# Kernel tuning notes

Hardware: AMD Instinct MI355X
Metric: run time of the kernel (lower is better)

## Reference

```python
import jax, jax.numpy as jnp
import numpy as np

N_NODES = 25000
IN_DIM = 16
EDGE_DIM = 8
HID = 32
OUT_DIM = 16
N_EDGES = 400000
MLP_HID = 32


def setup_inputs() -> dict:
    key = jax.random.key(0)
    ks = jax.random.split(key, 12)
    x = jax.random.normal(ks[0], (N_NODES, IN_DIM), dtype=jnp.float32)
    edge_index = jax.random.randint(ks[1], (2, N_EDGES), 0, N_NODES, dtype=jnp.int32)
    edge_attr = jax.random.normal(ks[2], (N_EDGES, EDGE_DIM), dtype=jnp.float32)
    s = lambda fan_in: 1.0 / np.sqrt(fan_in)
    W1 = jax.random.uniform(ks[3], (EDGE_DIM, MLP_HID), minval=-s(EDGE_DIM), maxval=s(EDGE_DIM))
    b1 = jax.random.uniform(ks[4], (MLP_HID,), minval=-s(EDGE_DIM), maxval=s(EDGE_DIM))
    W2 = jax.random.uniform(ks[5], (MLP_HID, IN_DIM * HID), minval=-s(MLP_HID), maxval=s(MLP_HID))
    b2 = jax.random.uniform(ks[6], (IN_DIM * HID,), minval=-s(MLP_HID), maxval=s(MLP_HID))
    root = jax.random.uniform(ks[7], (IN_DIM, HID), minval=-s(IN_DIM), maxval=s(IN_DIM))
    bias = jnp.zeros((HID,), dtype=jnp.float32)
    Wlin = jax.random.uniform(ks[8], (HID, OUT_DIM), minval=-s(HID), maxval=s(HID))
    blin = jax.random.uniform(ks[9], (OUT_DIM,), minval=-s(HID), maxval=s(HID))
    return {"x": x, "edge_attr": edge_attr, "W1": W1, "b1": b1, "W2": W2,
            "b2": b2, "root": root, "bias": bias, "Wlin": Wlin, "blin": blin,
            "edge_index": edge_index}


def reference(x, edge_attr, W1, b1, W2, b2, root, bias, Wlin, blin, edge_index):
    src, dst = edge_index[0], edge_index[1]  # x_j gathered from src, aggregated at dst
    # edge MLP -> per-edge weight matrix [E, IN_DIM, HID]
    h = jax.nn.relu(edge_attr @ W1 + b1)
    W_e = (h @ W2 + b2).reshape(-1, IN_DIM, HID)
    # gather source features and per-edge matvec: [E, HID]
    msg = jnp.einsum('ei,eio->eo', x[src], W_e)
    # scatter-mean over target nodes
    agg = jax.ops.segment_sum(msg, dst, num_segments=N_NODES)
    cnt = jax.ops.segment_sum(jnp.ones((msg.shape[0],), dtype=msg.dtype), dst, num_segments=N_NODES)
    agg = agg / jnp.maximum(cnt, 1.0)[:, None]
    # NNConv root weight + bias, then ReLU and final linear
    out = jax.nn.relu(agg + x @ root + bias)
    return out @ Wlin + blin
```

## Files before the change

### kernel.cpp

```cpp
#include <hip/hip_runtime.h>
#include <cstdint>

#define E_EDGES 400000
#define N_NODES 25000
#define NG      25000
#define NPACK   18432
#define EBLOCKS 782
#define NWAVES_E (EBLOCKS*4)

typedef float f32x4 __attribute__((ext_vector_type(4)));
typedef __bf16 bf16x8 __attribute__((ext_vector_type(8)));

static __device__ __forceinline__ ushort f2bf(float f) {
    union { __bf16 b; ushort u; } c; c.b = (__bf16)f; return c.u;
}

__global__ void __launch_bounds__(256) k_pack(const float* __restrict__ W2,
                                              const float* __restrict__ b2,
                                              const float* __restrict__ W1,
                                              const int* __restrict__ ei,
                                              ushort* __restrict__ packed,
                                              uint* __restrict__ cnt_u) {
    int t = blockIdx.x * 256 + threadIdx.x;
    if (t < NPACK) {
        float v = 0.0f;
        if (t < 17408) {
            int j  = t & 7;
            int ln = (t >> 3) & 15;
            int kg = (t >> 7) & 3;
            int nt = (t >> 9) & 1;
            int kt = t >> 10;
            int kap = (j < 4) ? (kg * 4 + j) : (16 + kg * 4 + (j - 4));
            if (kt < 16)       v = W2[kap * 512 + kt * 32 + nt * 16 + ln];
            else if (kap < 16) v = b2[kap * 32 + nt * 16 + ln];
        } else {
            int idx  = t - 17408;
            int half = idx >> 9;
            int lane = (idx >> 3) & 63;
            int j    = idx & 7;
            int kg = lane >> 4, ln = lane & 15;
            if (kg == 0) v = W1[j * 32 + half * 16 + ln];
        }
        packed[t] = f2bf(v);
    }
    if (t < E_EDGES) atomicAdd(&cnt_u[ei[E_EDGES + t]], 1u);
}

__global__ void __launch_bounds__(256, 2) k_edge(const float* __restrict__ ea,
                                                 const float* __restrict__ x,
                                                 const int* __restrict__ ei,
                                                 const ushort* __restrict__ packed,
                                                 const float* __restrict__ b1,
                                                 float* __restrict__ agg) {
    const int lane = threadIdx.x & 63;
    const int ln = lane & 15;
    const int kg = lane >> 4;
    const int wid = blockIdx.x * 4 + (threadIdx.x >> 6);

    bf16x8 wfr[34];
#pragma unroll
    for (int i = 0; i < 34; ++i)
        wfr[i] = *(const bf16x8*)(packed + (size_t)i * 512 + (size_t)lane * 8);
    const bf16x8 aw0 = *(const bf16x8*)(packed + 17408 + (size_t)lane * 8);
    const bf16x8 aw1 = *(const bf16x8*)(packed + 17408 + 512 + (size_t)lane * 8);
    const f32x4 blo4 = *(const f32x4*)(b1 + 4 * kg);
    const f32x4 bhi4 = *(const f32x4*)(b1 + 16 + 4 * kg);

    const f32x4 z4 = {0.f, 0.f, 0.f, 0.f};
    const __bf16 zb = (__bf16)0.0f;

    int g = wid;
    f32x4 ea0, ea1, xq0, xq1, xq2, xq3;
    {
        const int s0 = ei[g * 16 + ln];
        const f32x4* ep = (const f32x4*)(ea + (size_t)(g * 16 + ln) * 8);
        ea0 = ep[0]; ea1 = ep[1];
        const f32x4* xp = (const f32x4*)(x + (size_t)s0 * 16);
        xq0 = xp[0]; xq1 = xp[1]; xq2 = xp[2]; xq3 = xp[3];
    }

    while (true) {
        const int gn = g + NWAVES_E;
        const bool pf = gn < NG;

        int ns0 = 0;
        f32x4 nea0 = z4, nea1 = z4;
        if (pf) {
            ns0 = ei[gn * 16 + ln];
            const f32x4* nep = (const f32x4*)(ea + (size_t)(gn * 16 + ln) * 8);
            nea0 = nep[0]; nea1 = nep[1];
        }
        const int4 d4 = *(const int4*)(ei + E_EDGES + g * 16 + kg * 4);

        bf16x8 eb;
        if (kg == 0) {
            eb[0]=(__bf16)ea0[0]; eb[1]=(__bf16)ea0[1]; eb[2]=(__bf16)ea0[2]; eb[3]=(__bf16)ea0[3];
            eb[4]=(__bf16)ea1[0]; eb[5]=(__bf16)ea1[1]; eb[6]=(__bf16)ea1[2]; eb[7]=(__bf16)ea1[3];
        } else {
            eb[0]=zb; eb[1]=zb; eb[2]=zb; eb[3]=zb; eb[4]=zb; eb[5]=zb; eb[6]=zb; eb[7]=zb;
        }
        const f32x4 hA0 = __builtin_amdgcn_mfma_f32_16x16x32_bf16(aw0, eb, z4, 0, 0, 0);
        const f32x4 hA1 = __builtin_amdgcn_mfma_f32_16x16x32_bf16(aw1, eb, z4, 0, 0, 0);

        float h[8];
#pragma unroll
        for (int r = 0; r < 4; ++r) {
            h[r]     = fmaxf(hA0[r] + blo4[r], 0.f);
            h[4 + r] = fmaxf(hA1[r] + bhi4[r], 0.f);
        }

        float xr[16];
        xr[0]=xq0[0]; xr[1]=xq0[1]; xr[2]=xq0[2]; xr[3]=xq0[3];
        xr[4]=xq1[0]; xr[5]=xq1[1]; xr[6]=xq1[2]; xr[7]=xq1[3];
        xr[8]=xq2[0]; xr[9]=xq2[1]; xr[10]=xq2[2]; xr[11]=xq2[3];
        xr[12]=xq3[0]; xr[13]=xq3[1]; xr[14]=xq3[2]; xr[15]=xq3[3];

        f32x4 acc0 = z4, acc1 = z4;

#pragma unroll
        for (int kt = 0; kt < 8; ++kt) {
            const float xv = xr[kt];
            bf16x8 a;
#pragma unroll
            for (int j = 0; j < 8; ++j) a[j] = (__bf16)(xv * h[j]);
            acc0 = __builtin_amdgcn_mfma_f32_16x16x32_bf16(a, wfr[kt * 2 + 0], acc0, 0, 0, 0);
            acc1 = __builtin_amdgcn_mfma_f32_16x16x32_bf16(a, wfr[kt * 2 + 1], acc1, 0, 0, 0);
        }

        f32x4 nx0 = z4, nx1 = z4, nx2 = z4, nx3 = z4;
        if (pf) {
            const f32x4* nxp = (const f32x4*)(x + (size_t)ns0 * 16);
            nx0 = nxp[0]; nx1 = nxp[1]; nx2 = nxp[2]; nx3 = nxp[3];
        }

#pragma unroll
        for (int kt = 8; kt < 16; ++kt) {
            const float xv = xr[kt];
            bf16x8 a;
#pragma unroll
            for (int j = 0; j < 8; ++j) a[j] = (__bf16)(xv * h[j]);
            acc0 = __builtin_amdgcn_mfma_f32_16x16x32_bf16(a, wfr[kt * 2 + 0], acc0, 0, 0, 0);
            acc1 = __builtin_amdgcn_mfma_f32_16x16x32_bf16(a, wfr[kt * 2 + 1], acc1, 0, 0, 0);
        }
        {
            const f32x4 xs = (kg == 0) ? xq0 : ((kg == 1) ? xq1 : ((kg == 2) ? xq2 : xq3));
            bf16x8 a;
            a[0]=(__bf16)xs[0]; a[1]=(__bf16)xs[1]; a[2]=(__bf16)xs[2]; a[3]=(__bf16)xs[3];
            a[4]=zb; a[5]=zb; a[6]=zb; a[7]=zb;
            acc0 = __builtin_amdgcn_mfma_f32_16x16x32_bf16(a, wfr[32], acc0, 0, 0, 0);
            acc1 = __builtin_amdgcn_mfma_f32_16x16x32_bf16(a, wfr[33], acc1, 0, 0, 0);
        }

        atomicAdd(&agg[d4.x * 32 + ln],      acc0[0]);
        atomicAdd(&agg[d4.y * 32 + ln],      acc0[1]);
        atomicAdd(&agg[d4.z * 32 + ln],      acc0[2]);
        atomicAdd(&agg[d4.w * 32 + ln],      acc0[3]);
        atomicAdd(&agg[d4.x * 32 + 16 + ln], acc1[0]);
        atomicAdd(&agg[d4.y * 32 + 16 + ln], acc1[1]);
        atomicAdd(&agg[d4.z * 32 + 16 + ln], acc1[2]);
        atomicAdd(&agg[d4.w * 32 + 16 + ln], acc1[3]);

        if (!pf) break;
        g = gn;
        ea0 = nea0; ea1 = nea1;
        xq0 = nx0; xq1 = nx1; xq2 = nx2; xq3 = nx3;
    }
}

__global__ void __launch_bounds__(256) k_node(const float* __restrict__ agg,
                                              const uint* __restrict__ cnt_u,
                                              const float* __restrict__ x,
                                              const float* __restrict__ root,
                                              const float* __restrict__ bias,
                                              const float* __restrict__ Wlin,
                                              const float* __restrict__ blin,
                                              float* __restrict__ out) {
    __shared__ float al[256];
    const int n0 = blockIdx.x * 8;
    const int t = threadIdx.x;
    const int n = n0 + (t >> 5), h = t & 31;
    float a = 0.0f;
    if (n < N_NODES) {
        const float c = (float)cnt_u[n];
        float s = agg[n * 32 + h] / fmaxf(c, 1.0f) + bias[h];
        const f32x4* xp = (const f32x4*)(x + (size_t)n * 16);
        const f32x4 x0 = xp[0], x1 = xp[1], x2 = xp[2], x3 = xp[3];
        float xv[16];
        xv[0]=x0[0]; xv[1]=x0[1]; xv[2]=x0[2]; xv[3]=x0[3];
        xv[4]=x1[0]; xv[5]=x1[1]; xv[6]=x1[2]; xv[7]=x1[3];
        xv[8]=x2[0]; xv[9]=x2[1]; xv[10]=x2[2]; xv[11]=x2[3];
        xv[12]=x3[0]; xv[13]=x3[1]; xv[14]=x3[2]; xv[15]=x3[3];
#pragma unroll
        for (int i = 0; i < 16; ++i) s += xv[i] * root[i * 32 + h];
        a = fmaxf(s, 0.0f);
    }
    al[t] = a;
    __syncthreads();
    if (t < 128) {
        const int nj = n0 + (t >> 4), j = t & 15;
        if (nj < N_NODES) {
            float s = blin[j];
#pragma unroll
            for (int h2 = 0; h2 < 32; ++h2) s += al[(t >> 4) * 32 + h2] * Wlin[h2 * 16 + j];
            out[nj * 16 + j] = s;
        }
    }
}

extern "C" void kernel_launch(void* const* d_in, const int* in_sizes, int n_in,
                              void* d_out, int out_size, void* d_ws, size_t ws_size,
                              hipStream_t stream) {
    const float* x    = (const float*)d_in[0];
    const float* ea   = (const float*)d_in[1];
    const float* W1   = (const float*)d_in[2];
    const float* b1   = (const float*)d_in[3];
    const float* W2   = (const float*)d_in[4];
    const float* b2   = (const float*)d_in[5];
    const float* root = (const float*)d_in[6];
    const float* bias = (const float*)d_in[7];
    const float* Wlin = (const float*)d_in[8];
    const float* blin = (const float*)d_in[9];
    const int*   ei   = (const int*)d_in[10];
    float* out = (float*)d_out;

    char* ws = (char*)d_ws;
    float*  agg    = (float*)(ws + 0);
    uint*   cnt_u  = (uint*)(ws + 3200000);
    ushort* packed = (ushort*)(ws + 3300000);

    hipMemsetAsync(d_ws, 0, 3300000, stream);

    k_pack<<<1563, 256, 0, stream>>>(W2, b2, W1, ei, packed, cnt_u);
    k_edge<<<EBLOCKS, 256, 0, stream>>>(ea, x, ei, packed, b1, agg);
    k_node<<<3125, 256, 0, stream>>>(agg, cnt_u, x, root, bias, Wlin, blin, out);
}
```

Before: 87.18 us.

## Switch edge kernel to 32x32x16 MFMA with LDS-resident packed weights

Reworks the edge kernel so each wave handles 32 edges per iteration using 32x32x16 bf16 MFMAs instead of pairs of 16x16x32 MFMAs over 16 edges. The packed W2/b2 fragments now sit in shared memory instead of 34 register-held fragments, and the source-index prefetch is deepened by one more iteration. The aim is to cut MFMA instruction count, relieve register pressure, and hide gather latency better. In exchange it adds LDS reads inside the inner loop and a per-block LDS fill, changes the block count and launch bounds, and needs a matching repack of the weights.

```diff
diff --git a/kernel.cpp b/kernel.cpp
--- a/kernel.cpp
+++ b/kernel.cpp
@@ -3,12 +3,16 @@
 
 #define E_EDGES 400000
 #define N_NODES 25000
-#define NG      25000
-#define NPACK   18432
-#define EBLOCKS 782
-#define NWAVES_E (EBLOCKS*4)
-
-typedef float f32x4 __attribute__((ext_vector_type(4)));
+#define NG32    12500
+#define NTILES  33
+#define NPACKB  (NTILES*64*8)
+#define NPACKA  512
+#define NPACKT  (NPACKB+NPACKA)
+#define EBLOCKS 1042
+#define ESTRIDE (EBLOCKS*4)
+
+typedef float  f32x4  __attribute__((ext_vector_type(4)));
+typedef float  f32x16 __attribute__((ext_vector_type(16)));
 typedef __bf16 bf16x8 __attribute__((ext_vector_type(8)));
 
 static __device__ __forceinline__ ushort f2bf(float f) {
@@ -22,92 +26,118 @@
                                               ushort* __restrict__ packed,
                                               uint* __restrict__ cnt_u) {
     int t = blockIdx.x * 256 + threadIdx.x;
-    if (t < NPACK) {
+    if (t < NPACKT) {
         float v = 0.0f;
-        if (t < 17408) {
-            int j  = t & 7;
-            int ln = (t >> 3) & 15;
-            int kg = (t >> 7) & 3;
-            int nt = (t >> 9) & 1;
-            int kt = t >> 10;
-            int kap = (j < 4) ? (kg * 4 + j) : (16 + kg * 4 + (j - 4));
-            if (kt < 16)       v = W2[kap * 512 + kt * 32 + nt * 16 + ln];
-            else if (kap < 16) v = b2[kap * 32 + nt * 16 + ln];
+        if (t < NPACKB) {
+            int j = t & 7, lane = (t >> 3) & 63, kt = t >> 9;
+            int o = lane & 31, hi = lane >> 5;
+            if (kt < 32) {
+                int i = kt >> 1, p = kt & 1;
+                int m = (j & 3) + 8 * (2 * p + (j >> 2)) + 4 * hi;
+                v = W2[m * 512 + i * 32 + o];
+            } else {
+                int k = hi * 8 + j;
+                v = b2[k * 32 + o];
+            }
         } else {
-            int idx  = t - 17408;
-            int half = idx >> 9;
-            int lane = (idx >> 3) & 63;
-            int j    = idx & 7;
-            int kg = lane >> 4, ln = lane & 15;
-            if (kg == 0) v = W1[j * 32 + half * 16 + ln];
+            int t2 = t - NPACKB;
+            int j = t2 & 7, lane = t2 >> 3;
+            int m = lane & 31, hi = lane >> 5;
+            if (hi == 0) v = W1[j * 32 + m];
         }
         packed[t] = f2bf(v);
     }
     if (t < E_EDGES) atomicAdd(&cnt_u[ei[E_EDGES + t]], 1u);
 }
 
-__global__ void __launch_bounds__(256, 2) k_edge(const float* __restrict__ ea,
-                                                 const float* __restrict__ x,
-                                                 const int* __restrict__ ei,
-                                                 const ushort* __restrict__ packed,
-                                                 const float* __restrict__ b1,
-                                                 float* __restrict__ agg) {
+__global__ void __launch_bounds__(256) k_edge(const float* __restrict__ ea,
+                                              const float* __restrict__ x,
+                                              const int* __restrict__ ei,
+                                              const ushort* __restrict__ packed,
+                                              const float* __restrict__ b1,
+                                              float* __restrict__ agg) {
+    __shared__ alignas(16) ushort bl[NPACKB];
+    {
+        const uint4* s = (const uint4*)packed;
+        uint4* d = (uint4*)bl;
+        for (int i = threadIdx.x; i < NPACKB / 8; i += 256) d[i] = s[i];
+    }
+    __syncthreads();
+
     const int lane = threadIdx.x & 63;
-    const int ln = lane & 15;
-    const int kg = lane >> 4;
+    const int o  = lane & 31;
+    const int hi = lane >> 5;
     const int wid = blockIdx.x * 4 + (threadIdx.x >> 6);
 
-    bf16x8 wfr[34];
-#pragma unroll
-    for (int i = 0; i < 34; ++i)
-        wfr[i] = *(const bf16x8*)(packed + (size_t)i * 512 + (size_t)lane * 8);
-    const bf16x8 aw0 = *(const bf16x8*)(packed + 17408 + (size_t)lane * 8);
-    const bf16x8 aw1 = *(const bf16x8*)(packed + 17408 + 512 + (size_t)lane * 8);
-    const f32x4 blo4 = *(const f32x4*)(b1 + 4 * kg);
-    const f32x4 bhi4 = *(const f32x4*)(b1 + 16 + 4 * kg);
-
-    const f32x4 z4 = {0.f, 0.f, 0.f, 0.f};
+    const bf16x8 aw = *(const bf16x8*)(packed + NPACKB + (size_t)lane * 8);
+    const f32x4 b1q0 = *(const f32x4*)(b1 + 0  + 4 * hi);
+    const f32x4 b1q1 = *(const f32x4*)(b1 + 8  + 4 * hi);
+    const f32x4 b1q2 = *(const f32x4*)(b1 + 16 + 4 * hi);
+    const f32x4 b1q3 = *(const f32x4*)(b1 + 24 + 4 * hi);
+
+    const f32x16 z16 = {0.f,0.f,0.f,0.f,0.f,0.f,0.f,0.f,0.f,0.f,0.f,0.f,0.f,0.f,0.f,0.f};
+    const f32x4  z4  = {0.f,0.f,0.f,0.f};
     const __bf16 zb = (__bf16)0.0f;
 
     int g = wid;
     f32x4 ea0, ea1, xq0, xq1, xq2, xq3;
+    int s_nxt = 0;
     {
-        const int s0 = ei[g * 16 + ln];
-        const f32x4* ep = (const f32x4*)(ea + (size_t)(g * 16 + ln) * 8);
+        const int e = g * 32 + o;
+        const int s_cur = ei[e];
+        const f32x4* ep = (const f32x4*)(ea + (size_t)e * 8);
         ea0 = ep[0]; ea1 = ep[1];
-        const f32x4* xp = (const f32x4*)(x + (size_t)s0 * 16);
+        const f32x4* xp = (const f32x4*)(x + (size_t)s_cur * 16);
         xq0 = xp[0]; xq1 = xp[1]; xq2 = xp[2]; xq3 = xp[3];
+        const int gnx = g + ESTRIDE;
+        if (gnx < NG32) s_nxt = ei[gnx * 32 + o];
     }
 
     while (true) {
-        const int gn = g + NWAVES_E;
-        const bool pf = gn < NG;
-
-        int ns0 = 0;
-        f32x4 nea0 = z4, nea1 = z4;
+        const int gn = g + ESTRIDE;
+        const bool pf = gn < NG32;
+
+        f32x4 nea0 = z4, nea1 = z4, nx0 = z4, nx1 = z4, nx2 = z4, nx3 = z4;
+        int s_nn = 0;
         if (pf) {
-            ns0 = ei[gn * 16 + ln];
-            const f32x4* nep = (const f32x4*)(ea + (size_t)(gn * 16 + ln) * 8);
+            const f32x4* nep = (const f32x4*)(ea + (size_t)(gn * 32 + o) * 8);
             nea0 = nep[0]; nea1 = nep[1];
-        }
-        const int4 d4 = *(const int4*)(ei + E_EDGES + g * 16 + kg * 4);
+            const f32x4* nxp = (const f32x4*)(x + (size_t)s_nxt * 16);
+            nx0 = nxp[0]; nx1 = nxp[1]; nx2 = nxp[2]; nx3 = nxp[3];
+            const int gnn = gn + ESTRIDE;
+            if (gnn < NG32) s_nn = ei[gnn * 32 + o];
+        }
+        const int4 dq0 = *(const int4*)(ei + E_EDGES + g * 32 + 0  + 4 * hi);
+        const int4 dq1 = *(const int4*)(ei + E_EDGES + g * 32 + 8  + 4 * hi);
+        const int4 dq2 = *(const int4*)(ei + E_EDGES + g * 32 + 16 + 4 * hi);
+        const int4 dq3 = *(const int4*)(ei + E_EDGES + g * 32 + 24 + 4 * hi);
 
         bf16x8 eb;
-        if (kg == 0) {
+        if (hi == 0) {
             eb[0]=(__bf16)ea0[0]; eb[1]=(__bf16)ea0[1]; eb[2]=(__bf16)ea0[2]; eb[3]=(__bf16)ea0[3];
             eb[4]=(__bf16)ea1[0]; eb[5]=(__bf16)ea1[1]; eb[6]=(__bf16)ea1[2]; eb[7]=(__bf16)ea1[3];
         } else {
             eb[0]=zb; eb[1]=zb; eb[2]=zb; eb[3]=zb; eb[4]=zb; eb[5]=zb; eb[6]=zb; eb[7]=zb;
         }
-        const f32x4 hA0 = __builtin_amdgcn_mfma_f32_16x16x32_bf16(aw0, eb, z4, 0, 0, 0);
-        const f32x4 hA1 = __builtin_amdgcn_mfma_f32_16x16x32_bf16(aw1, eb, z4, 0, 0, 0);
-
-        float h[8];
-#pragma unroll
-        for (int r = 0; r < 4; ++r) {
-            h[r]     = fmaxf(hA0[r] + blo4[r], 0.f);
-            h[4 + r] = fmaxf(hA1[r] + bhi4[r], 0.f);
-        }
+        const f32x16 hC = __builtin_amdgcn_mfma_f32_32x32x16_bf16(aw, eb, z16, 0, 0, 0);
+
+        float hreg[16];
+        hreg[0]  = fmaxf(hC[0]  + b1q0[0], 0.f);
+        hreg[1]  = fmaxf(hC[1]  + b1q0[1], 0.f);
+        hreg[2]  = fmaxf(hC[2]  + b1q0[2], 0.f);
+        hreg[3]  = fmaxf(hC[3]  + b1q0[3], 0.f);
+        hreg[4]  = fmaxf(hC[4]  + b1q1[0], 0.f);
+        hreg[5]  = fmaxf(hC[5]  + b1q1[1], 0.f);
+        hreg[6]  = fmaxf(hC[6]  + b1q1[2], 0.f);
+        hreg[7]  = fmaxf(hC[7]  + b1q1[3], 0.f);
+        hreg[8]  = fmaxf(hC[8]  + b1q2[0], 0.f);
+        hreg[9]  = fmaxf(hC[9]  + b1q2[1], 0.f);
+        hreg[10] = fmaxf(hC[10] + b1q2[2], 0.f);
+        hreg[11] = fmaxf(hC[11] + b1q2[3], 0.f);
+        hreg[12] = fmaxf(hC[12] + b1q3[0], 0.f);
+        hreg[13] = fmaxf(hC[13] + b1q3[1], 0.f);
+        hreg[14] = fmaxf(hC[14] + b1q3[2], 0.f);
+        hreg[15] = fmaxf(hC[15] + b1q3[3], 0.f);
 
         float xr[16];
         xr[0]=xq0[0]; xr[1]=xq0[1]; xr[2]=xq0[2]; xr[3]=xq0[3];
@@ -115,55 +145,48 @@
         xr[8]=xq2[0]; xr[9]=xq2[1]; xr[10]=xq2[2]; xr[11]=xq2[3];
         xr[12]=xq3[0]; xr[13]=xq3[1]; xr[14]=xq3[2]; xr[15]=xq3[3];
 
-        f32x4 acc0 = z4, acc1 = z4;
-
-#pragma unroll
-        for (int kt = 0; kt < 8; ++kt) {
-            const float xv = xr[kt];
+        f32x16 acc = z16;
+
+#pragma unroll
+        for (int kt = 0; kt < 32; ++kt) {
+            const int p = kt & 1;
+            const float xv = xr[kt >> 1];
             bf16x8 a;
 #pragma unroll
-            for (int j = 0; j < 8; ++j) a[j] = (__bf16)(xv * h[j]);
-            acc0 = __builtin_amdgcn_mfma_f32_16x16x32_bf16(a, wfr[kt * 2 + 0], acc0, 0, 0, 0);
-            acc1 = __builtin_amdgcn_mfma_f32_16x16x32_bf16(a, wfr[kt * 2 + 1], acc1, 0, 0, 0);
-        }
-
-        f32x4 nx0 = z4, nx1 = z4, nx2 = z4, nx3 = z4;
-        if (pf) {
-            const f32x4* nxp = (const f32x4*)(x + (size_t)ns0 * 16);
-            nx0 = nxp[0]; nx1 = nxp[1]; nx2 = nxp[2]; nx3 = nxp[3];
-        }
-
-#pragma unroll
-        for (int kt = 8; kt < 16; ++kt) {
-            const float xv = xr[kt];
+            for (int j = 0; j < 8; ++j) a[j] = (__bf16)(xv * hreg[p * 8 + j]);
+            const bf16x8 bf = *(const bf16x8*)(&bl[kt * 512 + lane * 8]);
+            acc = __builtin_amdgcn_mfma_f32_32x32x16_bf16(a, bf, acc, 0, 0, 0);
+        }
+        {
             bf16x8 a;
 #pragma unroll
-            for (int j = 0; j < 8; ++j) a[j] = (__bf16)(xv * h[j]);
-            acc0 = __builtin_amdgcn_mfma_f32_16x16x32_bf16(a, wfr[kt * 2 + 0], acc0, 0, 0, 0);
-            acc1 = __builtin_amdgcn_mfma_f32_16x16x32_bf16(a, wfr[kt * 2 + 1], acc1, 0, 0, 0);
-        }
-        {
-            const f32x4 xs = (kg == 0) ? xq0 : ((kg == 1) ? xq1 : ((kg == 2) ? xq2 : xq3));
-            bf16x8 a;
-            a[0]=(__bf16)xs[0]; a[1]=(__bf16)xs[1]; a[2]=(__bf16)xs[2]; a[3]=(__bf16)xs[3];
-            a[4]=zb; a[5]=zb; a[6]=zb; a[7]=zb;
-            acc0 = __builtin_amdgcn_mfma_f32_16x16x32_bf16(a, wfr[32], acc0, 0, 0, 0);
-            acc1 = __builtin_amdgcn_mfma_f32_16x16x32_bf16(a, wfr[33], acc1, 0, 0, 0);
-        }
-
-        atomicAdd(&agg[d4.x * 32 + ln],      acc0[0]);
-        atomicAdd(&agg[d4.y * 32 + ln],      acc0[1]);
-        atomicAdd(&agg[d4.z * 32 + ln],      acc0[2]);
-        atomicAdd(&agg[d4.w * 32 + ln],      acc0[3]);
-        atomicAdd(&agg[d4.x * 32 + 16 + ln], acc1[0]);
-        atomicAdd(&agg[d4.y * 32 + 16 + ln], acc1[1]);
-        atomicAdd(&agg[d4.z * 32 + 16 + ln], acc1[2]);
-        atomicAdd(&agg[d4.w * 32 + 16 + ln], acc1[3]);
+            for (int j = 0; j < 8; ++j) a[j] = (__bf16)(hi ? xr[8 + j] : xr[j]);
+            const bf16x8 bf = *(const bf16x8*)(&bl[32 * 512 + lane * 8]);
+            acc = __builtin_amdgcn_mfma_f32_32x32x16_bf16(a, bf, acc, 0, 0, 0);
+        }
+
+        atomicAdd(&agg[dq0.x * 32 + o], acc[0]);
+        atomicAdd(&agg[dq0.y * 32 + o], acc[1]);
+        atomicAdd(&agg[dq0.z * 32 + o], acc[2]);
+        atomicAdd(&agg[dq0.w * 32 + o], acc[3]);
+        atomicAdd(&agg[dq1.x * 32 + o], acc[4]);
+        atomicAdd(&agg[dq1.y * 32 + o], acc[5]);
+        atomicAdd(&agg[dq1.z * 32 + o], acc[6]);
+        atomicAdd(&agg[dq1.w * 32 + o], acc[7]);
+        atomicAdd(&agg[dq2.x * 32 + o], acc[8]);
+        atomicAdd(&agg[dq2.y * 32 + o], acc[9]);
+        atomicAdd(&agg[dq2.z * 32 + o], acc[10]);
+        atomicAdd(&agg[dq2.w * 32 + o], acc[11]);
+        atomicAdd(&agg[dq3.x * 32 + o], acc[12]);
+        atomicAdd(&agg[dq3.y * 32 + o], acc[13]);
+        atomicAdd(&agg[dq3.z * 32 + o], acc[14]);
+        atomicAdd(&agg[dq3.w * 32 + o], acc[15]);
 
         if (!pf) break;
         g = gn;
         ea0 = nea0; ea1 = nea1;
         xq0 = nx0; xq1 = nx1; xq2 = nx2; xq3 = nx3;
+        s_nxt = s_nn;
     }
 }
 
```

Result: slower. 94.68 us (+8.6%).

## Stage packed W2 fragments in LDS and deepen the source-index prefetch pipeline

Applied to the files above, without the earlier changes.

The 34 per-lane bf16x8 weight fragments (136 VGPRs) are no longer held in registers. Each block copies the packed W2 matrix (about 34 KB) into shared memory once and reads the fragments from LDS inside the MFMA loop. Launch bounds rise from 2 to 4 blocks per SM and the grid grows to 1024 blocks, so more waves can be resident to hide gather and atomic latency. The source index is now prefetched two iterations ahead so the x gather is issued earlier. The cost is 34 LDS reads per iteration and an LDS budget that may limit occupancy (4 blocks need about 136 KB).

```diff
diff --git a/kernel.cpp b/kernel.cpp
--- a/kernel.cpp
+++ b/kernel.cpp
@@ -5,10 +5,10 @@
 #define N_NODES 25000
 #define NG      25000
 #define NPACK   18432
-#define EBLOCKS 782
-#define NWAVES_E (EBLOCKS*4)
-
-typedef float f32x4 __attribute__((ext_vector_type(4)));
+#define EBLOCKS 1024
+#define ESTRIDE (EBLOCKS*4)
+
+typedef float  f32x4  __attribute__((ext_vector_type(4)));
 typedef __bf16 bf16x8 __attribute__((ext_vector_type(8)));
 
 static __device__ __forceinline__ ushort f2bf(float f) {
@@ -46,21 +46,25 @@
     if (t < E_EDGES) atomicAdd(&cnt_u[ei[E_EDGES + t]], 1u);
 }
 
-__global__ void __launch_bounds__(256, 2) k_edge(const float* __restrict__ ea,
+__global__ void __launch_bounds__(256, 4) k_edge(const float* __restrict__ ea,
                                                  const float* __restrict__ x,
                                                  const int* __restrict__ ei,
                                                  const ushort* __restrict__ packed,
                                                  const float* __restrict__ b1,
                                                  float* __restrict__ agg) {
+    __shared__ alignas(16) ushort w2l[17408];
+    {
+        const uint4* s = (const uint4*)packed;
+        uint4* d = (uint4*)w2l;
+        for (int i = threadIdx.x; i < 2176; i += 256) d[i] = s[i];
+    }
+    __syncthreads();
+
     const int lane = threadIdx.x & 63;
     const int ln = lane & 15;
     const int kg = lane >> 4;
     const int wid = blockIdx.x * 4 + (threadIdx.x >> 6);
 
-    bf16x8 wfr[34];
-#pragma unroll
-    for (int i = 0; i < 34; ++i)
-        wfr[i] = *(const bf16x8*)(packed + (size_t)i * 512 + (size_t)lane * 8);
     const bf16x8 aw0 = *(const bf16x8*)(packed + 17408 + (size_t)lane * 8);
     const bf16x8 aw1 = *(const bf16x8*)(packed + 17408 + 512 + (size_t)lane * 8);
     const f32x4 blo4 = *(const f32x4*)(b1 + 4 * kg);
@@ -70,32 +74,38 @@
     const __bf16 zb = (__bf16)0.0f;
 
     int g = wid;
-    f32x4 ea0, ea1, xq0, xq1, xq2, xq3;
+    f32x4 eac0, eac1, xc0, xc1, xc2, xc3;
+    int s_nx = 0;
     {
         const int s0 = ei[g * 16 + ln];
         const f32x4* ep = (const f32x4*)(ea + (size_t)(g * 16 + ln) * 8);
-        ea0 = ep[0]; ea1 = ep[1];
+        eac0 = ep[0]; eac1 = ep[1];
         const f32x4* xp = (const f32x4*)(x + (size_t)s0 * 16);
-        xq0 = xp[0]; xq1 = xp[1]; xq2 = xp[2]; xq3 = xp[3];
+        xc0 = xp[0]; xc1 = xp[1]; xc2 = xp[2]; xc3 = xp[3];
+        const int g1 = g + ESTRIDE;
+        if (g1 < NG) s_nx = ei[g1 * 16 + ln];
     }
 
     while (true) {
-        const int gn = g + NWAVES_E;
+        const int gn = g + ESTRIDE;
         const bool pf = gn < NG;
 
-        int ns0 = 0;
-        f32x4 nea0 = z4, nea1 = z4;
+        f32x4 ean0 = z4, ean1 = z4, xn0 = z4, xn1 = z4, xn2 = z4, xn3 = z4;
+        int s_nx2 = 0;
         if (pf) {
-            ns0 = ei[gn * 16 + ln];
             const f32x4* nep = (const f32x4*)(ea + (size_t)(gn * 16 + ln) * 8);
-            nea0 = nep[0]; nea1 = nep[1];
+            ean0 = nep[0]; ean1 = nep[1];
+            const f32x4* nxp = (const f32x4*)(x + (size_t)s_nx * 16);
+            xn0 = nxp[0]; xn1 = nxp[1]; xn2 = nxp[2]; xn3 = nxp[3];
+            const int gnn = gn + ESTRIDE;
+            if (gnn < NG) s_nx2 = ei[gnn * 16 + ln];
         }
         const int4 d4 = *(const int4*)(ei + E_EDGES + g * 16 + kg * 4);
 
         bf16x8 eb;
         if (kg == 0) {
-            eb[0]=(__bf16)ea0[0]; eb[1]=(__bf16)ea0[1]; eb[2]=(__bf16)ea0[2]; eb[3]=(__bf16)ea0[3];
-            eb[4]=(__bf16)ea1[0]; eb[5]=(__bf16)ea1[1]; eb[6]=(__bf16)ea1[2]; eb[7]=(__bf16)ea1[3];
+            eb[0]=(__bf16)eac0[0]; eb[1]=(__bf16)eac0[1]; eb[2]=(__bf16)eac0[2]; eb[3]=(__bf16)eac0[3];
+            eb[4]=(__bf16)eac1[0]; eb[5]=(__bf16)eac1[1]; eb[6]=(__bf16)eac1[2]; eb[7]=(__bf16)eac1[3];
         } else {
             eb[0]=zb; eb[1]=zb; eb[2]=zb; eb[3]=zb; eb[4]=zb; eb[5]=zb; eb[6]=zb; eb[7]=zb;
         }
@@ -110,45 +120,33 @@
         }
 
         float xr[16];
-        xr[0]=xq0[0]; xr[1]=xq0[1]; xr[2]=xq0[2]; xr[3]=xq0[3];
-        xr[4]=xq1[0]; xr[5]=xq1[1]; xr[6]=xq1[2]; xr[7]=xq1[3];
-        xr[8]=xq2[0]; xr[9]=xq2[1]; xr[10]=xq2[2]; xr[11]=xq2[3];
-        xr[12]=xq3[0]; xr[13]=xq3[1]; xr[14]=xq3[2]; xr[15]=xq3[3];
+        xr[0]=xc0[0]; xr[1]=xc0[1]; xr[2]=xc0[2]; xr[3]=xc0[3];
+        xr[4]=xc1[0]; xr[5]=xc1[1]; xr[6]=xc1[2]; xr[7]=xc1[3];
+        xr[8]=xc2[0]; xr[9]=xc2[1]; xr[10]=xc2[2]; xr[11]=xc2[3];
+        xr[12]=xc3[0]; xr[13]=xc3[1]; xr[14]=xc3[2]; xr[15]=xc3[3];
 
         f32x4 acc0 = z4, acc1 = z4;
 
 #pragma unroll
-        for (int kt = 0; kt < 8; ++kt) {
+        for (int kt = 0; kt < 16; ++kt) {
             const float xv = xr[kt];
             bf16x8 a;
 #pragma unroll
             for (int j = 0; j < 8; ++j) a[j] = (__bf16)(xv * h[j]);
-            acc0 = __builtin_amdgcn_mfma_f32_16x16x32_bf16(a, wfr[kt * 2 + 0], acc0, 0, 0, 0);
-            acc1 = __builtin_amdgcn_mfma_f32_16x16x32_bf16(a, wfr[kt * 2 + 1], acc1, 0, 0, 0);
-        }
-
-        f32x4 nx0 = z4, nx1 = z4, nx2 = z4, nx3 = z4;
-        if (pf) {
-            const f32x4* nxp = (const f32x4*)(x + (size_t)ns0 * 16);
-            nx0 = nxp[0]; nx1 = nxp[1]; nx2 = nxp[2]; nx3 = nxp[3];
-        }
-
-#pragma unroll
-        for (int kt = 8; kt < 16; ++kt) {
-            const float xv = xr[kt];
-            bf16x8 a;
-#pragma unroll
-            for (int j = 0; j < 8; ++j) a[j] = (__bf16)(xv * h[j]);
-            acc0 = __builtin_amdgcn_mfma_f32_16x16x32_bf16(a, wfr[kt * 2 + 0], acc0, 0, 0, 0);
-            acc1 = __builtin_amdgcn_mfma_f32_16x16x32_bf16(a, wfr[kt * 2 + 1], acc1, 0, 0, 0);
+            const bf16x8 bf0 = *(const bf16x8*)(&w2l[(kt * 2 + 0) * 512 + lane * 8]);
+            const bf16x8 bf1 = *(const bf16x8*)(&w2l[(kt * 2 + 1) * 512 + lane * 8]);
+            acc0 = __builtin_amdgcn_mfma_f32_16x16x32_bf16(a, bf0, acc0, 0, 0, 0);
+            acc1 = __builtin_amdgcn_mfma_f32_16x16x32_bf16(a, bf1, acc1, 0, 0, 0);
         }
         {
-            const f32x4 xs = (kg == 0) ? xq0 : ((kg == 1) ? xq1 : ((kg == 2) ? xq2 : xq3));
+            const f32x4 xs = (kg == 0) ? xc0 : ((kg == 1) ? xc1 : ((kg == 2) ? xc2 : xc3));
             bf16x8 a;
             a[0]=(__bf16)xs[0]; a[1]=(__bf16)xs[1]; a[2]=(__bf16)xs[2]; a[3]=(__bf16)xs[3];
             a[4]=zb; a[5]=zb; a[6]=zb; a[7]=zb;
-            acc0 = __builtin_amdgcn_mfma_f32_16x16x32_bf16(a, wfr[32], acc0, 0, 0, 0);
-            acc1 = __builtin_amdgcn_mfma_f32_16x16x32_bf16(a, wfr[33], acc1, 0, 0, 0);
+            const bf16x8 bf0 = *(const bf16x8*)(&w2l[(16 * 2 + 0) * 512 + lane * 8]);
+            const bf16x8 bf1 = *(const bf16x8*)(&w2l[(16 * 2 + 1) * 512 + lane * 8]);
+            acc0 = __builtin_amdgcn_mfma_f32_16x16x32_bf16(a, bf0, acc0, 0, 0, 0);
+            acc1 = __builtin_amdgcn_mfma_f32_16x16x32_bf16(a, bf1, acc1, 0, 0, 0);
         }
 
         atomicAdd(&agg[d4.x * 32 + ln],      acc0[0]);
@@ -162,8 +160,9 @@
 
         if (!pf) break;
         g = gn;
-        ea0 = nea0; ea1 = nea1;
-        xq0 = nx0; xq1 = nx1; xq2 = nx2; xq3 = nx3;
+        eac0 = ean0; eac1 = ean1;
+        xc0 = xn0; xc1 = xn1; xc2 = xn2; xc3 = xn3;
+        s_nx = s_nx2;
     }
 }
 
```

Measured after the change: 161.0 us. +84.7%, slower.
